# Optimization experiments

Measured on AMD Instinct MI355X. Metric: run time of the kernel, lower is better.

The kernel has to match this reference:

```python
import jax, jax.numpy as jnp
import numpy as np


def gcn_conv(x, edge_index, edge_weight, W, b):
    """PyG GCNConv: add self-loops (weight 1), symmetric normalization,
    linear transform, edge-weighted scatter-add aggregation, bias."""
    N = x.shape[0]
    src = jnp.concatenate([edge_index[0], jnp.arange(N, dtype=edge_index.dtype)])
    dst = jnp.concatenate([edge_index[1], jnp.arange(N, dtype=edge_index.dtype)])
    ew = jnp.concatenate([edge_weight, jnp.ones((N,), dtype=edge_weight.dtype)])
    # deg over destination nodes (source_to_target flow)
    deg = jax.ops.segment_sum(ew, dst, num_segments=N)
    dinv = jnp.where(deg > 0, deg ** -0.5, 0.0).astype(x.dtype)
    norm = dinv[src] * ew * dinv[dst]          # [E+N]
    xw = x @ W                                  # [N, out] linear first (cheaper)
    msgs = norm[:, None] * xw[src]              # [E+N, out]
    out = jax.ops.segment_sum(msgs, dst, num_segments=N)
    return out + b


def setup_inputs() -> dict:
    key = jax.random.key(0)
    ks = jax.random.split(key, 7)
    N, E, F_in, H, F_out = 100000, 1600000, 394, 256, 64
    x = jax.random.normal(ks[0], (N, F_in), dtype=jnp.float32)
    edge_index = jax.random.randint(ks[1], (2, E), 0, N, dtype=jnp.int32)
    edge_weight = jax.random.uniform(ks[2], (E,), dtype=jnp.float32)
    W1 = jax.random.normal(ks[3], (F_in, H), dtype=jnp.float32) * (1.0 / np.sqrt(F_in))
    b1 = jnp.zeros((H,), dtype=jnp.float32)
    W2 = jax.random.normal(ks[4], (H, F_out), dtype=jnp.float32) * (1.0 / np.sqrt(H))
    b2 = jnp.zeros((F_out,), dtype=jnp.float32)
    return {"x": x, "edge_index": edge_index, "edge_weight": edge_weight,
            "W1": W1, "b1": b1, "W2": W2, "b2": b2}


def reference(x, edge_index, edge_weight, W1, b1, W2, b2):
    h = gcn_conv(x, edge_index, edge_weight, W1, b1)
    h = jax.nn.relu(h)
    # F.dropout(training=self.training) is identity in eval mode
    out = gcn_conv(h, edge_index, edge_weight, W2, b2)
    return out
```

## Files before the change

### kernel.cpp

```cpp
#include <hip/hip_runtime.h>
#include <hip/hip_bf16.h>
#include <hip/hip_fp16.h>
#include <type_traits>


typedef _Float16 f16x8 __attribute__((ext_vector_type(8)));
typedef float f32x4 __attribute__((ext_vector_type(4)));

#define DEG_MASK ((1ull << 42) - 1)

__device__ inline void async_copy16(const void* g, void* l) {
    __builtin_amdgcn_global_load_lds(
        (const __attribute__((address_space(1))) void*)g,
        (__attribute__((address_space(3))) void*)l, 16, 0, 0);
}


__global__ __launch_bounds__(256) void init_node(unsigned long long* packed, int N) {
    int i = blockIdx.x * 256 + threadIdx.x;
    if (i < N) packed[i] = 0ull;
}

__global__ __launch_bounds__(256) void accum_deg_hist(const int* __restrict__ dst,
                                                      const float* __restrict__ ew,
                                                      unsigned long long* packed, int E) {
    int e = blockIdx.x * 256 + threadIdx.x;
    if (e < E) {
        int d = dst[e];
        unsigned long long add =
            (1ull << 42) + (unsigned long long)(ew[e] * 4294967296.0f);
        atomicAdd(&packed[d], add);
    }
}

#define SCAN_TILE 2048

__global__ __launch_bounds__(256) void scan1(const unsigned long long* __restrict__ packed,
                                             int* __restrict__ rowptr,
                                             float* __restrict__ dinv,
                                             int* __restrict__ bsums, int N) {
    __shared__ int tmp[256];
    int t = threadIdx.x;
    int base = blockIdx.x * SCAN_TILE + t * 8;
    int v[8], s = 0;
#pragma unroll
    for (int j = 0; j < 8; ++j) {
        int idx = base + j;
        if (idx < N) {
            unsigned long long pv = packed[idx];
            v[j] = (int)(pv >> 42);
            dinv[idx] = rsqrtf(1.0f + (float)(pv & DEG_MASK) * (1.0f / 4294967296.0f));
        } else v[j] = 0;
        s += v[j];
    }
    tmp[t] = s;
    __syncthreads();
#pragma unroll
    for (int off = 1; off < 256; off <<= 1) {
        int u = (t >= off) ? tmp[t - off] : 0;
        __syncthreads();
        tmp[t] += u;
        __syncthreads();
    }
    int run = tmp[t] - s;
#pragma unroll
    for (int j = 0; j < 8; ++j) {
        if (base + j < N) rowptr[base + j] = run;
        run += v[j];
    }
    if (t == 255) bsums[blockIdx.x] = tmp[255];
}

__global__ __launch_bounds__(256) void scan2(int* bsums, int* rowptr, int NB, int N, int E) {
    __shared__ int tmp[256];
    int t = threadIdx.x;
    int v = (t < NB) ? bsums[t] : 0;
    tmp[t] = v;
    __syncthreads();
#pragma unroll
    for (int off = 1; off < 256; off <<= 1) {
        int u = (t >= off) ? tmp[t - off] : 0;
        __syncthreads();
        tmp[t] += u;
        __syncthreads();
    }
    if (t < NB) bsums[t] = tmp[t] - v;
    if (t == 0) rowptr[N] = E;
}

__global__ __launch_bounds__(256) void scan3(int* rowptr, int* cursor,
                                             const int* __restrict__ bsums, int N) {
    int base = blockIdx.x * SCAN_TILE + threadIdx.x * 8;
    int off = bsums[blockIdx.x];
#pragma unroll
    for (int j = 0; j < 8; ++j)
        if (base + j < N) {
            int v = rowptr[base + j] + off;
            rowptr[base + j] = v;
            cursor[base + j] = v;
        }
}

__global__ __launch_bounds__(256) void fill_csr(const int* __restrict__ src,
                                                const int* __restrict__ dst,
                                                const float* __restrict__ ew,
                                                const float* __restrict__ dinv,
                                                int* __restrict__ cursor,
                                                int2* __restrict__ cv, int E) {
    int e = blockIdx.x * 256 + threadIdx.x;
    if (e < E) {
        int d = dst[e], s = src[e];
        int pos = atomicAdd(&cursor[d], 1);
        float v = dinv[s] * ew[e];
        cv[pos] = make_int2(s, __float_as_int(v));
    }
}

__global__ __launch_bounds__(256) void tohalf_w(const float* __restrict__ W,
                                                __half* __restrict__ WT,
                                                int K, int N, int Kpad) {
    int idx = blockIdx.x * 256 + threadIdx.x;
    int total = N * Kpad;
    if (idx >= total) return;
    int n = idx / Kpad, k = idx % Kpad;
    float v = (k < K) ? W[(size_t)k * N + n] : 0.0f;
    WT[idx] = __float2half(v);
}

template <int BM, int BN, int WARPS_M, int WARPS_N, int NT>
__global__ __launch_bounds__(NT) void gemm_f32a(const float* __restrict__ Ax,
                                                const __half* __restrict__ BT,
                                                __half* __restrict__ C,
                                                int M, int K, int Kpad) {
    const int WM = BM / WARPS_M, WN = BN / WARPS_N;
    const int FM = WM / 16, FN = WN / 16;
    const int ACH = BM * 4;
    const int BCH = BN * 4;
    static_assert(ACH == NT, "1 A-chunk per thread");
    static_assert(BCH == 2 * NT, "2 B-chunks per thread");
    __shared__ __align__(16) __half lds[2][(ACH + BCH) * 8];

    int tid = threadIdx.x;
    int lane = tid & 63;
    int w = tid >> 6;
    int wr = w / WARPS_N, wc = w % WARPS_N;
    int bm = blockIdx.x * BM;
    int lrow = lane & 15;
    int lslot = lane >> 4;

    int arow = tid >> 2, ap = tid & 3;
    int aslot = ap ^ ((arow >> 1) & 3);
    int agrow = bm + arow; if (agrow >= M) agrow = M - 1;
    const float* abase = Ax + (size_t)agrow * K;

    const __half* bsrc[2];
#pragma unroll
    for (int i = 0; i < 2; ++i) {
        int c = tid + i * NT;
        int row = c >> 2, p = c & 3;
        bsrc[i] = BT + (size_t)row * Kpad + (size_t)((p ^ ((row >> 1) & 3)) * 8);
    }

    f32x4 acc[FM][FN];
#pragma unroll
    for (int m = 0; m < FM; ++m)
#pragma unroll
        for (int n = 0; n < FN; ++n) acc[m][n] = (f32x4){0.f, 0.f, 0.f, 0.f};

    float2 ar[4];
    auto loadA = [&](int s) {
        int gk = s * 32 + aslot * 8;
        if (gk + 8 <= K) {
            const float* p = abase + gk;
            ar[0] = *(const float2*)p;
            ar[1] = *(const float2*)(p + 2);
            ar[2] = *(const float2*)(p + 4);
            ar[3] = *(const float2*)(p + 6);
        } else {
            float t[8];
#pragma unroll
            for (int j = 0; j < 8; ++j) t[j] = (gk + j < K) ? abase[gk + j] : 0.0f;
            ar[0] = make_float2(t[0], t[1]);
            ar[1] = make_float2(t[2], t[3]);
            ar[2] = make_float2(t[4], t[5]);
            ar[3] = make_float2(t[6], t[7]);
        }
    };
    auto writeA = [&](int buf) {
        union { __half2 h[4]; uint4 u; } pk;
#pragma unroll
        for (int j = 0; j < 4; ++j) pk.h[j] = __floats2half2_rn(ar[j].x, ar[j].y);
        *(uint4*)&lds[buf][(size_t)tid * 8] = pk.u;
    };
    auto stageB = [&](int buf) {
#pragma unroll
        for (int i = 0; i < 2; ++i) {
            async_copy16(bsrc[i], &lds[buf][(size_t)((tid & ~63) + (i + 1) * NT) * 8]);
            bsrc[i] += 32;
        }
    };

    auto compute = [&](int buf) {
        f16x8 af[FM], bf[FN];
#pragma unroll
        for (int m = 0; m < FM; ++m) {
            int row = wr * WM + m * 16 + lrow;
            int p = lslot ^ ((row >> 1) & 3);
            af[m] = *(const f16x8*)&lds[buf][(size_t)(row * 4 + p) * 8];
        }
#pragma unroll
        for (int n = 0; n < FN; ++n) {
            int row = wc * WN + n * 16 + lrow;
            int p = lslot ^ ((row >> 1) & 3);
            bf[n] = *(const f16x8*)&lds[buf][(size_t)(ACH + row * 4 + p) * 8];
        }
#pragma unroll
        for (int m = 0; m < FM; ++m)
#pragma unroll
            for (int n = 0; n < FN; ++n)
                acc[m][n] = __builtin_amdgcn_mfma_f32_16x16x32_f16(af[m], bf[n], acc[m][n], 0, 0, 0);
    };

    const int nsteps = Kpad / 32;
    loadA(0);
    stageB(0);
    asm volatile("s_waitcnt vmcnt(2)" ::: "memory");
    writeA(0);
    asm volatile("s_waitcnt vmcnt(0) lgkmcnt(0)" ::: "memory");
    __builtin_amdgcn_s_barrier();
    for (int s = 0; s < nsteps; ++s) {
        bool more = (s + 1 < nsteps);
        if (more) { loadA(s + 1); stageB((s + 1) & 1); }
        compute(s & 1);
        if (more) {
            asm volatile("s_waitcnt vmcnt(2)" ::: "memory");
            writeA((s + 1) & 1);
            asm volatile("s_waitcnt vmcnt(0) lgkmcnt(0)" ::: "memory");
        }
        __builtin_amdgcn_s_barrier();
    }

    __syncthreads();
    {
        const int LW = WN + 8;
        __half* tile = (__half*)lds + (size_t)w * 16 * LW;
        const int CPR = WN / 8;
        const int CHT = (16 * CPR) / 64;
#pragma unroll
        for (int m = 0; m < FM; ++m) {
            int rb = bm + wr * WM + m * 16;
#pragma unroll
            for (int n = 0; n < FN; ++n)
#pragma unroll
                for (int i = 0; i < 4; ++i)
                    tile[((lane >> 4) * 4 + i) * LW + n * 16 + (lane & 15)] =
                        __float2half(acc[m][n][i]);
#pragma unroll
            for (int c = 0; c < CHT; ++c) {
                int ch = lane + c * 64;
                int r = ch / CPR, cc = ch % CPR;
                uint4 v = *(uint4*)&tile[r * LW + cc * 8];
                int grow = rb + r;
                if (grow < M)
                    *(uint4*)&C[(size_t)grow * BN + wc * WN + cc * 8] = v;
            }
        }
    }
}

template <int BM, int BN, int WARPS_M, int WARPS_N, int NT>
__global__ __launch_bounds__(NT) void gemm_f16(const __half* __restrict__ Ah,
                                               const __half* __restrict__ BT,
                                               __half* __restrict__ C,
                                               int M, int Kpad) {
    const int WM = BM / WARPS_M, WN = BN / WARPS_N;
    const int FM = WM / 16, FN = WN / 16;
    const int ACH = BM * 4;
    const int BCH = BN * 4;
    const int TOTCH = ACH + BCH;
    const int CH = TOTCH / NT;
    static_assert(CH == 3, "vmcnt(3) hardcoded below");
    __shared__ __align__(16) __half lds[2][TOTCH * 8];

    int tid = threadIdx.x;
    int lane = tid & 63;
    int w = tid >> 6;
    int wr = w / WARPS_N, wc = w % WARPS_N;
    int bm = blockIdx.x * BM;
    int lrow = lane & 15;
    int lslot = lane >> 4;

    const __half* srcp[CH];
#pragma unroll
    for (int i = 0; i < CH; ++i) {
        int ch = tid + i * NT;
        if (ch < ACH) {
            int c = ch, row = c >> 2;
            int grow = bm + row;
            if (grow >= M) grow = M - 1;
            srcp[i] = Ah + (size_t)grow * Kpad + (size_t)(((c & 3) ^ ((row >> 1) & 3)) * 8);
        } else {
            int c = ch - ACH, row = c >> 2;
            srcp[i] = BT + (size_t)row * Kpad + (size_t)(((c & 3) ^ ((row >> 1) & 3)) * 8);
        }
    }

    f32x4 acc[FM][FN];
#pragma unroll
    for (int m = 0; m < FM; ++m)
#pragma unroll
        for (int n = 0; n < FN; ++n) acc[m][n] = (f32x4){0.f, 0.f, 0.f, 0.f};

    auto stage = [&](int buf) {
#pragma unroll
        for (int i = 0; i < CH; ++i) {
            async_copy16(srcp[i], &lds[buf][(size_t)((tid & ~63) + i * NT) * 8]);
            srcp[i] += 32;
        }
    };

    auto compute = [&](int buf) {
        f16x8 af[FM], bf[FN];
#pragma unroll
        for (int m = 0; m < FM; ++m) {
            int row = wr * WM + m * 16 + lrow;
            int p = lslot ^ ((row >> 1) & 3);
            af[m] = *(const f16x8*)&lds[buf][(size_t)(row * 4 + p) * 8];
        }
#pragma unroll
        for (int n = 0; n < FN; ++n) {
            int row = wc * WN + n * 16 + lrow;
            int p = lslot ^ ((row >> 1) & 3);
            bf[n] = *(const f16x8*)&lds[buf][(size_t)(ACH + row * 4 + p) * 8];
        }
#pragma unroll
        for (int m = 0; m < FM; ++m)
#pragma unroll
            for (int n = 0; n < FN; ++n)
                acc[m][n] = __builtin_amdgcn_mfma_f32_16x16x32_f16(af[m], bf[n], acc[m][n], 0, 0, 0);
    };

    const int nsteps = Kpad / 32;
    stage(0);
    for (int s = 0; s < nsteps; ++s) {
        if (s + 1 < nsteps) {
            stage((s + 1) & 1);
            asm volatile("s_waitcnt vmcnt(3)" ::: "memory");
        } else {
            asm volatile("s_waitcnt vmcnt(0)" ::: "memory");
        }
        __builtin_amdgcn_s_barrier();
        compute(s & 1);
        __builtin_amdgcn_s_barrier();
    }

    __syncthreads();
    {
        const int LW = WN + 8;
        __half* tile = (__half*)lds + (size_t)w * 16 * LW;
        const int CPR = WN / 8;
        const int CHT = (16 * CPR) / 64;
#pragma unroll
        for (int m = 0; m < FM; ++m) {
            int rb = bm + wr * WM + m * 16;
#pragma unroll
            for (int n = 0; n < FN; ++n)
#pragma unroll
                for (int i = 0; i < 4; ++i)
                    tile[((lane >> 4) * 4 + i) * LW + n * 16 + (lane & 15)] =
                        __float2half(acc[m][n][i]);
#pragma unroll
            for (int c = 0; c < CHT; ++c) {
                int ch = lane + c * 64;
                int r = ch / CPR, cc = ch % CPR;
                uint4 v = *(uint4*)&tile[r * LW + cc * 8];
                int grow = rb + r;
                if (grow < M)
                    *(uint4*)&C[(size_t)grow * BN + wc * WN + cc * 8] = v;
            }
        }
    }
}

template <int F, int LPN, int RELU, typename OutT>
__global__ __launch_bounds__(256) void gatherh(const int* __restrict__ rowptr,
                                               const int2* __restrict__ cv,
                                               const __half* __restrict__ xw,
                                               const float* __restrict__ dinv,
                                               const float* __restrict__ bias,
                                               OutT* __restrict__ out, int N) {
    const int NPB = 256 / LPN;
    int d = blockIdx.x * NPB + threadIdx.x / LPN;
    if (d >= N) return;
    int lane = threadIdx.x % LPN;

    float di = dinv[d];
    uint2 raw = *(const uint2*)(xw + (size_t)d * F + lane * 4);
    float2 u0 = __half22float2(*(__half2*)&raw.x);
    float2 u1 = __half22float2(*(__half2*)&raw.y);
    float a0 = di * u0.x, a1 = di * u0.y, a2 = di * u1.x, a3 = di * u1.y;
    float b0 = 0.f, b1 = 0.f, b2 = 0.f, b3 = 0.f;

    int p = rowptr[d], p1 = rowptr[d + 1];
    for (; p + 4 <= p1; p += 4) {
        int2 e0 = cv[p], e1 = cv[p + 1], e2 = cv[p + 2], e3 = cv[p + 3];
        uint2 r0 = *(const uint2*)(xw + (size_t)e0.x * F + lane * 4);
        uint2 r1 = *(const uint2*)(xw + (size_t)e1.x * F + lane * 4);
        uint2 r2 = *(const uint2*)(xw + (size_t)e2.x * F + lane * 4);
        uint2 r3 = *(const uint2*)(xw + (size_t)e3.x * F + lane * 4);
        float w0 = __int_as_float(e0.y), w1 = __int_as_float(e1.y);
        float w2 = __int_as_float(e2.y), w3 = __int_as_float(e3.y);
        {
            float2 v0 = __half22float2(*(__half2*)&r0.x);
            float2 v1 = __half22float2(*(__half2*)&r0.y);
            a0 = fmaf(w0, v0.x, a0); a1 = fmaf(w0, v0.y, a1);
            a2 = fmaf(w0, v1.x, a2); a3 = fmaf(w0, v1.y, a3);
        }
        {
            float2 v0 = __half22float2(*(__half2*)&r1.x);
            float2 v1 = __half22float2(*(__half2*)&r1.y);
            b0 = fmaf(w1, v0.x, b0); b1 = fmaf(w1, v0.y, b1);
            b2 = fmaf(w1, v1.x, b2); b3 = fmaf(w1, v1.y, b3);
        }
        {
            float2 v0 = __half22float2(*(__half2*)&r2.x);
            float2 v1 = __half22float2(*(__half2*)&r2.y);
            a0 = fmaf(w2, v0.x, a0); a1 = fmaf(w2, v0.y, a1);
            a2 = fmaf(w2, v1.x, a2); a3 = fmaf(w2, v1.y, a3);
        }
        {
            float2 v0 = __half22float2(*(__half2*)&r3.x);
            float2 v1 = __half22float2(*(__half2*)&r3.y);
            b0 = fmaf(w3, v0.x, b0); b1 = fmaf(w3, v0.y, b1);
            b2 = fmaf(w3, v1.x, b2); b3 = fmaf(w3, v1.y, b3);
        }
    }
    for (; p < p1; ++p) {
        int2 e = cv[p];
        float wv = __int_as_float(e.y);
        uint2 rv = *(const uint2*)(xw + (size_t)e.x * F + lane * 4);
        float2 v0 = __half22float2(*(__half2*)&rv.x);
        float2 v1 = __half22float2(*(__half2*)&rv.y);
        a0 = fmaf(wv, v0.x, a0); a1 = fmaf(wv, v0.y, a1);
        a2 = fmaf(wv, v1.x, a2); a3 = fmaf(wv, v1.y, a3);
    }
    a0 += b0; a1 += b1; a2 += b2; a3 += b3;
    a0 *= di; a1 *= di; a2 *= di; a3 *= di;

    float4 bb = *(const float4*)&bias[lane * 4];
    a0 += bb.x; a1 += bb.y; a2 += bb.z; a3 += bb.w;
    if (RELU) {
        a0 = fmaxf(a0, 0.f); a1 = fmaxf(a1, 0.f);
        a2 = fmaxf(a2, 0.f); a3 = fmaxf(a3, 0.f);
    }
    if constexpr (std::is_same_v<OutT, float>) {
        *(float4*)&out[(size_t)d * F + lane * 4] = make_float4(a0, a1, a2, a3);
    } else {
        __half2 h0 = __floats2half2_rn(a0, a1);
        __half2 h1 = __floats2half2_rn(a2, a3);
        uint2 packed;
        packed.x = *(uint*)&h0;
        packed.y = *(uint*)&h1;
        *(uint2*)&out[(size_t)d * F + lane * 4] = packed;
    }
}

extern "C" void kernel_launch(void* const* d_in, const int* in_sizes, int n_in,
                              void* d_out, int out_size, void* d_ws, size_t ws_size,
                              hipStream_t stream) {
    const float* x  = (const float*)d_in[0];
    const int*   ei = (const int*)d_in[1];
    const float* ew = (const float*)d_in[2];
    const float* W1 = (const float*)d_in[3];
    const float* b1 = (const float*)d_in[4];
    const float* W2 = (const float*)d_in[5];
    const float* b2 = (const float*)d_in[6];
    float* out = (float*)d_out;

    const int H    = in_sizes[4];
    const int Fout = in_sizes[6];
    const int Fin  = in_sizes[3] / H;
    const int N    = in_sizes[0] / Fin;
    const int E    = in_sizes[2];

    const int Kpad1 = (Fin + 31) / 32 * 32;
    const int Kpad2 = (H + 31) / 32 * 32;

    const int* src = ei;
    const int* dst = ei + E;

    unsigned long long* packed = (unsigned long long*)d_ws;
    float* dinv   = (float*)(packed + N);
    int*   rowptr = (int*)(dinv + N);
    int*   cursor = rowptr + N + 4;
    int*   bsums  = cursor + N + 4;
    int2*  cv     = (int2*)(bsums + 256);
    __half* bufA  = (__half*)(cv + E);
    __half* bufB  = bufA + (size_t)N * H;
    __half* wt1   = bufB + (size_t)N * H;
    __half* wt2   = wt1 + (size_t)H * Kpad1;

    const int NB = (N + SCAN_TILE - 1) / SCAN_TILE;

    init_node<<<(N + 255) / 256, 256, 0, stream>>>(packed, N);
    accum_deg_hist<<<(E + 255) / 256, 256, 0, stream>>>(dst, ew, packed, E);

    scan1<<<NB, 256, 0, stream>>>(packed, rowptr, dinv, bsums, N);
    scan2<<<1, 256, 0, stream>>>(bsums, rowptr, NB, N, E);
    scan3<<<NB, 256, 0, stream>>>(rowptr, cursor, bsums, N);
    fill_csr<<<(E + 255) / 256, 256, 0, stream>>>(src, dst, ew, dinv, cursor, cv, E);

    tohalf_w<<<(H * Kpad1 + 255) / 256, 256, 0, stream>>>(W1, wt1, Fin, H, Kpad1);
    tohalf_w<<<(Fout * Kpad2 + 255) / 256, 256, 0, stream>>>(W2, wt2, H, Fout, Kpad2);

    gemm_f32a<128, 256, 2, 4, 512><<<(N + 127) / 128, 512, 0, stream>>>(
        x, wt1, bufA, N, Fin, Kpad1);

    gatherh<256, 64, 1, __half><<<(N + 3) / 4, 256, 0, stream>>>(
        rowptr, cv, bufA, dinv, b1, bufB, N);

    gemm_f16<128, 64, 2, 2, 256><<<(N + 127) / 128, 256, 0, stream>>>(bufB, wt2, bufA, N, Kpad2);

    gatherh<64, 16, 0, float><<<(N + 15) / 16, 256, 0, stream>>>(
        rowptr, cv, bufA, dinv, b2, out, N);
}
```

Baseline: 466.6 us.

## Merge setup kernels and co-schedule CSR fill with first GEMM

Folds node-buffer zeroing and both weight transposes/half conversions into one setup launch. Merges the CSR fill (atomic scatter of edges) into the first GEMM launch as extra leading blocks, so the latency-bound atomic scatter can overlap with the compute-heavy GEMM. This cuts several launches and idle gaps. The cost is that fill blocks carry the GEMM's LDS allocation and 512-thread shape, which may limit occupancy for those blocks.

```diff
diff --git a/kernel.cpp b/kernel.cpp
--- a/kernel.cpp
+++ b/kernel.cpp
@@ -16,9 +16,35 @@
 }
 
 
-__global__ __launch_bounds__(256) void init_node(unsigned long long* packed, int N) {
-    int i = blockIdx.x * 256 + threadIdx.x;
-    if (i < N) packed[i] = 0ull;
+__global__ __launch_bounds__(256) void setup(unsigned long long* packed, int N,
+                                             const float* __restrict__ W1,
+                                             __half* __restrict__ WT1,
+                                             int K1, int N1, int Kpad1,
+                                             const float* __restrict__ W2,
+                                             __half* __restrict__ WT2,
+                                             int K2, int N2, int Kpad2,
+                                             int G0, int G1) {
+    int b = blockIdx.x;
+    if (b < G0) {
+        int i = b * 256 + threadIdx.x;
+        if (i < N) packed[i] = 0ull;
+    } else if (b < G1) {
+        int idx = (b - G0) * 256 + threadIdx.x;
+        int total = N1 * Kpad1;
+        if (idx < total) {
+            int n = idx / Kpad1, k = idx % Kpad1;
+            float v = (k < K1) ? W1[(size_t)k * N1 + n] : 0.0f;
+            WT1[idx] = __float2half(v);
+        }
+    } else {
+        int idx = (b - G1) * 256 + threadIdx.x;
+        int total = N2 * Kpad2;
+        if (idx < total) {
+            int n = idx / Kpad2, k = idx % Kpad2;
+            float v = (k < K2) ? W2[(size_t)k * N2 + n] : 0.0f;
+            WT2[idx] = __float2half(v);
+        }
+    }
 }
 
 __global__ __launch_bounds__(256) void accum_deg_hist(const int* __restrict__ dst,
@@ -101,37 +127,18 @@
         }
 }
 
-__global__ __launch_bounds__(256) void fill_csr(const int* __restrict__ src,
-                                                const int* __restrict__ dst,
-                                                const float* __restrict__ ew,
-                                                const float* __restrict__ dinv,
-                                                int* __restrict__ cursor,
-                                                int2* __restrict__ cv, int E) {
-    int e = blockIdx.x * 256 + threadIdx.x;
-    if (e < E) {
-        int d = dst[e], s = src[e];
-        int pos = atomicAdd(&cursor[d], 1);
-        float v = dinv[s] * ew[e];
-        cv[pos] = make_int2(s, __float_as_int(v));
-    }
-}
-
-__global__ __launch_bounds__(256) void tohalf_w(const float* __restrict__ W,
-                                                __half* __restrict__ WT,
-                                                int K, int N, int Kpad) {
-    int idx = blockIdx.x * 256 + threadIdx.x;
-    int total = N * Kpad;
-    if (idx >= total) return;
-    int n = idx / Kpad, k = idx % Kpad;
-    float v = (k < K) ? W[(size_t)k * N + n] : 0.0f;
-    WT[idx] = __float2half(v);
-}
-
 template <int BM, int BN, int WARPS_M, int WARPS_N, int NT>
-__global__ __launch_bounds__(NT) void gemm_f32a(const float* __restrict__ Ax,
-                                                const __half* __restrict__ BT,
-                                                __half* __restrict__ C,
-                                                int M, int K, int Kpad) {
+__global__ __launch_bounds__(NT) void gemm1_fill(const float* __restrict__ Ax,
+                                                 const __half* __restrict__ BT,
+                                                 __half* __restrict__ C,
+                                                 int M, int K, int Kpad,
+                                                 int GF,
+                                                 const int* __restrict__ src,
+                                                 const int* __restrict__ dst,
+                                                 const float* __restrict__ ew,
+                                                 const float* __restrict__ dinv,
+                                                 int* __restrict__ cursor,
+                                                 int2* __restrict__ cv, int E) {
     const int WM = BM / WARPS_M, WN = BN / WARPS_N;
     const int FM = WM / 16, FN = WN / 16;
     const int ACH = BM * 4;
@@ -140,11 +147,22 @@
     static_assert(BCH == 2 * NT, "2 B-chunks per thread");
     __shared__ __align__(16) __half lds[2][(ACH + BCH) * 8];
 
+    if ((int)blockIdx.x < GF) {
+        int e = blockIdx.x * NT + threadIdx.x;
+        if (e < E) {
+            int d = dst[e], s = src[e];
+            int pos = atomicAdd(&cursor[d], 1);
+            float v = dinv[s] * ew[e];
+            cv[pos] = make_int2(s, __float_as_int(v));
+        }
+        return;
+    }
+
     int tid = threadIdx.x;
     int lane = tid & 63;
     int w = tid >> 6;
     int wr = w / WARPS_N, wc = w % WARPS_N;
-    int bm = blockIdx.x * BM;
+    int bm = (blockIdx.x - GF) * BM;
     int lrow = lane & 15;
     int lslot = lane >> 4;
 
@@ -502,19 +520,29 @@
 
     const int NB = (N + SCAN_TILE - 1) / SCAN_TILE;
 
-    init_node<<<(N + 255) / 256, 256, 0, stream>>>(packed, N);
+    {
+        int g0 = (N + 255) / 256;
+        int g1 = (H * Kpad1 + 255) / 256;
+        int g2 = (Fout * Kpad2 + 255) / 256;
+        setup<<<g0 + g1 + g2, 256, 0, stream>>>(packed, N,
+                                                W1, wt1, Fin, H, Kpad1,
+                                                W2, wt2, H, Fout, Kpad2,
+                                                g0, g0 + g1);
+    }
+
     accum_deg_hist<<<(E + 255) / 256, 256, 0, stream>>>(dst, ew, packed, E);
 
     scan1<<<NB, 256, 0, stream>>>(packed, rowptr, dinv, bsums, N);
     scan2<<<1, 256, 0, stream>>>(bsums, rowptr, NB, N, E);
     scan3<<<NB, 256, 0, stream>>>(rowptr, cursor, bsums, N);
-    fill_csr<<<(E + 255) / 256, 256, 0, stream>>>(src, dst, ew, dinv, cursor, cv, E);
-
-    tohalf_w<<<(H * Kpad1 + 255) / 256, 256, 0, stream>>>(W1, wt1, Fin, H, Kpad1);
-    tohalf_w<<<(Fout * Kpad2 + 255) / 256, 256, 0, stream>>>(W2, wt2, H, Fout, Kpad2);
-
-    gemm_f32a<128, 256, 2, 4, 512><<<(N + 127) / 128, 512, 0, stream>>>(
-        x, wt1, bufA, N, Fin, Kpad1);
+
+    {
+        int GF = (E + 511) / 512;
+        int G1 = (N + 127) / 128;
+        gemm1_fill<128, 256, 2, 4, 512><<<GF + G1, 512, 0, stream>>>(
+            x, wt1, bufA, N, Fin, Kpad1,
+            GF, src, dst, ew, dinv, cursor, cv, E);
+    }
 
     gatherh<256, 64, 1, __half><<<(N + 3) / 4, 256, 0, stream>>>(
         rowptr, cv, bufA, dinv, b1, bufB, N);
```

Result: faster. 450.4 us (-3.5%).
